# Performance work log

Measured on AMD Instinct MI355X. Metric: run time of the kernel, lower is better.

Reference implementation:

```python
import jax, jax.numpy as jnp
import numpy as np

N_NODES = 100_000
N_EDGES = 600_000
D = 128  # in_channels


def setup_inputs() -> dict:
    key = jax.random.key(0)
    k1, k2, k3, k4, k5 = jax.random.split(key, 5)
    node_embs_src = jax.random.normal(k1, (N_NODES, D), dtype=jnp.float32)
    node_embs_dst = jax.random.normal(k2, (N_NODES, D), dtype=jnp.float32)
    edge_index = jax.random.randint(k3, (2, N_EDGES), 0, N_NODES, dtype=jnp.int64)
    # MLP params: Linear(2D -> D), Linear(D -> 1); scaled like default torch init
    W1 = jax.random.normal(k4, (2 * D, D), dtype=jnp.float32) / np.sqrt(2 * D)
    b1 = jnp.zeros((D,), dtype=jnp.float32)
    W2 = jax.random.normal(k5, (D, 1), dtype=jnp.float32) / np.sqrt(D)
    b2 = jnp.zeros((1,), dtype=jnp.float32)
    return {
        "node_embs_src": node_embs_src,
        "node_embs_dst": node_embs_dst,
        "edge_index": edge_index,
        "W1": W1,
        "b1": b1,
        "W2": W2,
        "b2": b2,
    }


def reference(node_embs_src, node_embs_dst, edge_index, W1, b1, W2, b2):
    # Gather per-edge source / destination embeddings: [E, D] each
    src = node_embs_src[edge_index[0]]
    dst = node_embs_dst[edge_index[1]]
    # concat([src, dst]) @ W1 == src @ W1[:D] + dst @ W1[D:]  (avoids materializing [E, 2D])
    h = jnp.dot(src, W1[:D]) + jnp.dot(dst, W1[D:]) + b1  # [E, D]
    h = jax.nn.relu(h)
    logits = jnp.dot(h, W2) + b2  # [E, 1]
    return jax.nn.sigmoid(logits)
```

## Files before the change

kernel.cpp:

```cpp
#include <hip/hip_runtime.h>
#include <stdint.h>

typedef __attribute__((ext_vector_type(8))) short short8;
typedef __attribute__((ext_vector_type(8))) signed char schar8;
typedef __attribute__((ext_vector_type(4))) float f32x4;

__device__ __forceinline__ unsigned short f2bf(float f) {
  union { float f; uint32_t u; } v; v.f = f;
  uint32_t u = v.u;
  uint32_t r = (u + 0x7FFFu + ((u >> 16) & 1u)) >> 16;
  return (unsigned short)r;
}
__device__ __forceinline__ float bf2f(unsigned short h) {
  union { uint32_t u; float f; } v; v.u = ((uint32_t)h) << 16; return v.f;
}

#define NBM 64
__global__ __launch_bounds__(256, 3)
void node_phase_q8(const float* __restrict__ src_emb,
                   const float* __restrict__ dst_emb,
                   const float* __restrict__ W1,
                   const float* __restrict__ b1,
                   int8_t* __restrict__ Q,
                   float* __restrict__ SC,
                   int Nn, int ntiles) {
  __shared__ __align__(16) char Als[NBM * 256];
  __shared__ __align__(16) char Wlds[128 * 256];

  const int tbl = blockIdx.y;
  const float* emb = tbl ? dst_emb : src_emb;
  const float* Wt  = W1 + (size_t)tbl * 128 * 128;
  int8_t* Qt  = Q  + (size_t)tbl * Nn * 128;
  float*  SCt = SC + (size_t)tbl * Nn;

  const int tid  = threadIdx.x;
  const int lane = tid & 63;
  const int w    = tid >> 6;
  const int l15  = lane & 15;
  const int lg   = lane >> 4;

  for (int c = tid; c < 2048; c += 256) {
    const int col = c >> 4;
    const int k8  = (c & 15) * 8;
    short8 t;
#pragma unroll
    for (int j = 0; j < 8; ++j)
      t[j] = (short)f2bf(Wt[(size_t)(k8 + j) * 128 + col]);
    const int byteoff = (col * 256 + k8 * 2) ^ (((col >> 3) & 7) << 4);
    *(short8*)(Wlds + byteoff) = t;
  }

  float b1s[8];
#pragma unroll
  for (int j = 0; j < 8; ++j) b1s[j] = tbl ? 0.f : b1[l15 * 8 + j];

  const int q = tid & 15, r0 = tid >> 4;
  const int swzA = (l15 & 7) << 4;
  const int gx = gridDim.x;

  float4 p0[4], p1[4];
#pragma unroll
  for (int i = 0; i < 4; ++i) {
    const int node = blockIdx.x * NBM + i * 16 + r0;
    if (node < Nn) {
      const float* base = emb + (size_t)node * 128 + q * 8;
      p0[i] = *(const float4*)base;
      p1[i] = *(const float4*)(base + 4);
    }
  }

  for (int t = blockIdx.x; t < ntiles; t += gx) {
    const int t0 = t * NBM;

#pragma unroll
    for (int i = 0; i < 4; ++i) {
      const int row = i * 16 + r0;
      short8 hv;
      hv[0] = (short)f2bf(p0[i].x); hv[1] = (short)f2bf(p0[i].y);
      hv[2] = (short)f2bf(p0[i].z); hv[3] = (short)f2bf(p0[i].w);
      hv[4] = (short)f2bf(p1[i].x); hv[5] = (short)f2bf(p1[i].y);
      hv[6] = (short)f2bf(p1[i].z); hv[7] = (short)f2bf(p1[i].w);
      const int byteoff = row * 256 + ((q * 16) ^ ((row & 7) << 4));
      *(short8*)(Als + byteoff) = hv;
    }
    __syncthreads();

    const int tn = t + gx;
    if (tn < ntiles) {
#pragma unroll
      for (int i = 0; i < 4; ++i) {
        const int node = tn * NBM + i * 16 + r0;
        if (node < Nn) {
          const float* base = emb + (size_t)node * 128 + q * 8;
          p0[i] = *(const float4*)base;
          p1[i] = *(const float4*)(base + 4);
        }
      }
    }

    f32x4 acc[8];
#pragma unroll
    for (int cf = 0; cf < 8; ++cf) acc[cf] = (f32x4){0.f, 0.f, 0.f, 0.f};

#pragma unroll
    for (int s = 0; s < 4; ++s) {
      const int aoff = (w * 16 + l15) * 256 + ((s * 64 + lg * 16) ^ swzA);
      const short8 a = *(const short8*)(Als + aoff);
#pragma unroll
      for (int cf = 0; cf < 8; ++cf) {
        const int col = l15 * 8 + cf;
        const int boff = (col * 256 + s * 64 + lg * 16) ^ (((col >> 3) & 7) << 4);
        const short8 b = *(const short8*)(Wlds + boff);
        acc[cf] = __builtin_amdgcn_mfma_f32_16x16x32_bf16(a, b, acc[cf], 0, 0, 0);
      }
    }

#pragma unroll
    for (int reg = 0; reg < 4; ++reg) {
      float h[8];
      float am = 1e-20f;
#pragma unroll
      for (int cf = 0; cf < 8; ++cf) {
        h[cf] = acc[cf][reg] + b1s[cf];
        am = fmaxf(am, fabsf(h[cf]));
      }
      am = fmaxf(am, __shfl_xor(am, 1, 16));
      am = fmaxf(am, __shfl_xor(am, 2, 16));
      am = fmaxf(am, __shfl_xor(am, 4, 16));
      am = fmaxf(am, __shfl_xor(am, 8, 16));
      const int node = t0 + w * 16 + lg * 4 + reg;
      if (node < Nn) {
        const float rq = 127.0f / am;
        uint32_t lo = 0, hi = 0;
#pragma unroll
        for (int cf = 0; cf < 4; ++cf)
          lo |= ((uint32_t)((int)rintf(h[cf] * rq) & 255)) << (8 * cf);
#pragma unroll
        for (int cf = 4; cf < 8; ++cf)
          hi |= ((uint32_t)((int)rintf(h[cf] * rq) & 255)) << (8 * (cf - 4));
        uint2 pk; pk.x = lo; pk.y = hi;
        *(uint2*)(Qt + (size_t)node * 128 + l15 * 8) = pk;
        if (l15 == 0) SCt[node] = am * (1.0f / 127.0f);
      }
    }
    __syncthreads();
  }
}

__global__ __launch_bounds__(256, 8)
void edge_phase_q8(const int8_t* __restrict__ Qu,
                   const int8_t* __restrict__ Qv,
                   const float* __restrict__ scu,
                   const float* __restrict__ scv,
                   const int* __restrict__ eidx,
                   const float* __restrict__ W2,
                   const float* __restrict__ b2,
                   float* __restrict__ out,
                   int E) {
  const int tid = threadIdx.x;
  const int l15 = tid & 15;
  const int sg  = tid >> 4;

  float w2s[8];
#pragma unroll
  for (int j = 0; j < 8; ++j) w2s[j] = W2[l15 * 8 + j];
  const float b2s = b2[0];
  const int stride = gridDim.x * 16;

#pragma unroll 2
  for (int e = blockIdx.x * 16 + sg; e < E; e += stride) {
    const int s = eidx[e];
    const int d = eidx[E + e];
    const schar8 qu = *(const schar8*)(Qu + (size_t)s * 128 + l15 * 8);
    const schar8 qv = *(const schar8*)(Qv + (size_t)d * 128 + l15 * 8);
    const float su = scu[s];
    const float sv = scv[d];
    float acc = 0.f;
#pragma unroll
    for (int j = 0; j < 8; ++j) {
      float g = (float)(int)qu[j] * su + (float)(int)qv[j] * sv;
      g = g > 0.f ? g : 0.f;
      acc = fmaf(g, w2s[j], acc);
    }
    acc += __shfl_xor(acc, 1, 16);
    acc += __shfl_xor(acc, 2, 16);
    acc += __shfl_xor(acc, 4, 16);
    acc += __shfl_xor(acc, 8, 16);
    if (l15 == 0) out[e] = 1.f / (1.f + __expf(-(acc + b2s)));
  }
}

#define BM 64
__global__ __launch_bounds__(256, 4)
void edge_decoder_fused(const float* __restrict__ src_emb,
                        const float* __restrict__ dst_emb,
                        const int* __restrict__ eidx,
                        const float* __restrict__ W1,
                        const float* __restrict__ b1,
                        const float* __restrict__ W2,
                        const float* __restrict__ b2,
                        float* __restrict__ out,
                        int E, int ntiles) {
  __shared__ __align__(16) char Als[BM * 512];
  __shared__ float rowpart[4][BM];

  const int tid  = threadIdx.x;
  const int lane = tid & 63;
  const int w    = tid >> 6;
  const int l15  = lane & 15;
  const int lk8  = (lane >> 4) * 8;

  short8 bfrag[8][2];
#pragma unroll
  for (int s = 0; s < 8; ++s) {
#pragma unroll
    for (int nf = 0; nf < 2; ++nf) {
      const int col = w * 32 + nf * 16 + l15;
      short8 t;
#pragma unroll
      for (int j = 0; j < 8; ++j) {
        const int k = s * 32 + lk8 + j;
        t[j] = (short)f2bf(W1[k * 128 + col]);
      }
      bfrag[s][nf] = t;
    }
  }
  float b1v[2], w2v[2];
#pragma unroll
  for (int nf = 0; nf < 2; ++nf) {
    const int col = w * 32 + nf * 16 + l15;
    b1v[nf] = b1[col];
    w2v[nf] = W2[col];
  }
  const float b2s = b2[0];

  const int q  = tid & 31;
  const int r0 = tid >> 5;
  const int qq = q & 15;
  const bool is_src = (q < 16);
  const int swz = (l15 & 7) << 4;

  for (int t = blockIdx.x; t < ntiles; t += gridDim.x) {
    const int t0 = t * BM;
#pragma unroll
    for (int i = 0; i < 8; ++i) {
      const int row = i * 8 + r0;
      const int e = t0 + row;
      if (e < E) {
        const int node = is_src ? eidx[e] : eidx[E + e];
        const float* base = (is_src ? src_emb : dst_emb) + (size_t)node * 128 + qq * 8;
        const float4 f0 = *(const float4*)base;
        const float4 f1 = *(const float4*)(base + 4);
        short8 hv;
        hv[0] = (short)f2bf(f0.x); hv[1] = (short)f2bf(f0.y);
        hv[2] = (short)f2bf(f0.z); hv[3] = (short)f2bf(f0.w);
        hv[4] = (short)f2bf(f1.x); hv[5] = (short)f2bf(f1.y);
        hv[6] = (short)f2bf(f1.z); hv[7] = (short)f2bf(f1.w);
        const int byteoff = row * 512 + ((q * 16) ^ ((row & 7) << 4));
        *(short8*)(Als + byteoff) = hv;
      }
    }
    __syncthreads();

    for (int m = 0; m < 4; ++m) {
      f32x4 acc0 = {0.f, 0.f, 0.f, 0.f};
      f32x4 acc1 = {0.f, 0.f, 0.f, 0.f};
      const int rowb = (m * 16 + l15) * 512;
      const int kb0  = lk8 * 2;
#pragma unroll
      for (int s = 0; s < 8; ++s) {
        const int off = rowb + ((s * 64 + kb0) ^ swz);
        const short8 a = *(const short8*)(Als + off);
        acc0 = __builtin_amdgcn_mfma_f32_16x16x32_bf16(a, bfrag[s][0], acc0, 0, 0, 0);
        acc1 = __builtin_amdgcn_mfma_f32_16x16x32_bf16(a, bfrag[s][1], acc1, 0, 0, 0);
      }
      float pr[4];
#pragma unroll
      for (int reg = 0; reg < 4; ++reg) {
        float h0 = acc0[reg] + b1v[0]; h0 = h0 > 0.f ? h0 : 0.f;
        float h1 = acc1[reg] + b1v[1]; h1 = h1 > 0.f ? h1 : 0.f;
        pr[reg] = h0 * w2v[0] + h1 * w2v[1];
      }
#pragma unroll
      for (int off = 1; off < 16; off <<= 1) {
#pragma unroll
        for (int reg = 0; reg < 4; ++reg)
          pr[reg] += __shfl_xor(pr[reg], off, 64);
      }
      if (l15 == 0) {
        const int rbase = m * 16 + (lane >> 4) * 4;
#pragma unroll
        for (int reg = 0; reg < 4; ++reg)
          rowpart[w][rbase + reg] = pr[reg];
      }
    }
    __syncthreads();

    if (tid < BM) {
      const int e = t0 + tid;
      if (e < E) {
        const float sum = rowpart[0][tid] + rowpart[1][tid] +
                          rowpart[2][tid] + rowpart[3][tid] + b2s;
        out[e] = 1.f / (1.f + __expf(-sum));
      }
    }
    __syncthreads();
  }
}

extern "C" void kernel_launch(void* const* d_in, const int* in_sizes, int n_in,
                              void* d_out, int out_size, void* d_ws, size_t ws_size,
                              hipStream_t stream) {
  const float* src = (const float*)d_in[0];
  const float* dst = (const float*)d_in[1];
  const int*   eix = (const int*)d_in[2];
  const float* W1  = (const float*)d_in[3];
  const float* b1  = (const float*)d_in[4];
  const float* W2  = (const float*)d_in[5];
  const float* b2  = (const float*)d_in[6];
  float* out = (float*)d_out;

  const int E  = in_sizes[2] / 2;
  const int Nn = in_sizes[0] / 128;
  const size_t q_bytes  = (size_t)2 * Nn * 128;
  const size_t sc_bytes = (size_t)2 * Nn * sizeof(float);

  if (ws_size >= q_bytes + sc_bytes) {
    int8_t* Q  = (int8_t*)d_ws;
    float*  SC = (float*)((char*)d_ws + q_bytes);
    const int ntiles_n = (Nn + NBM - 1) / NBM;
    const int gx = ntiles_n < 384 ? ntiles_n : 384;
    node_phase_q8<<<dim3(gx, 2), 256, 0, stream>>>(src, dst, W1, b1, Q, SC, Nn, ntiles_n);
    const int nchunks = (E + 15) / 16;
    const int nblk = nchunks < 2048 ? nchunks : 2048;
    edge_phase_q8<<<nblk, 256, 0, stream>>>(Q, Q + (size_t)Nn * 128, SC, SC + Nn,
                                            eix, W2, b2, out, E);
  } else {
    const int ntiles = (E + BM - 1) / BM;
    const int grid = ntiles < 2048 ? ntiles : 2048;
    edge_decoder_fused<<<grid, 256, 0, stream>>>(src, dst, eix, W1, b1, W2, b2,
                                                 out, E, ntiles);
  }
}
```

Before: 75.62 us.

## Hold W1 fragments in registers, transpose MFMA roles, move bias to edge phase

The node-phase GEMM now keeps the bf16 W1 operand in per-wave registers (afrag) instead of LDS, swapping MFMA A/B roles so each lane owns one node row and writes contiguous 32-byte quantized chunks. Per-row absmax now needs only two cross-lane shuffles, and the LDS weight tile is gone, removing its per-iteration reads. The b1 bias moves out of the quantized node activations into the edge phase as an extra FMA. In exchange register pressure rises sharply (128 VGPRs of weights), so occupancy is lowered to 2 and the grid to 256 blocks per table. Quantization error shifts because the quantized values no longer include the bias.

```diff
diff --git a/kernel.cpp b/kernel.cpp
--- a/kernel.cpp
+++ b/kernel.cpp
@@ -16,16 +16,14 @@
 }
 
 #define NBM 64
-__global__ __launch_bounds__(256, 3)
+__global__ __launch_bounds__(256, 2)
 void node_phase_q8(const float* __restrict__ src_emb,
                    const float* __restrict__ dst_emb,
                    const float* __restrict__ W1,
-                   const float* __restrict__ b1,
                    int8_t* __restrict__ Q,
                    float* __restrict__ SC,
                    int Nn, int ntiles) {
   __shared__ __align__(16) char Als[NBM * 256];
-  __shared__ __align__(16) char Wlds[128 * 256];
 
   const int tbl = blockIdx.y;
   const float* emb = tbl ? dst_emb : src_emb;
@@ -39,23 +37,23 @@
   const int l15  = lane & 15;
   const int lg   = lane >> 4;
 
-  for (int c = tid; c < 2048; c += 256) {
-    const int col = c >> 4;
-    const int k8  = (c & 15) * 8;
-    short8 t;
-#pragma unroll
-    for (int j = 0; j < 8; ++j)
-      t[j] = (short)f2bf(Wt[(size_t)(k8 + j) * 128 + col]);
-    const int byteoff = (col * 256 + k8 * 2) ^ (((col >> 3) & 7) << 4);
-    *(short8*)(Wlds + byteoff) = t;
-  }
-
-  float b1s[8];
-#pragma unroll
-  for (int j = 0; j < 8; ++j) b1s[j] = tbl ? 0.f : b1[l15 * 8 + j];
+  const int pbase = (l15 >> 2) * 32 + (l15 & 3);
+  short8 afrag[8][4];
+#pragma unroll
+  for (int m = 0; m < 8; ++m) {
+#pragma unroll
+    for (int s = 0; s < 4; ++s) {
+      short8 t;
+#pragma unroll
+      for (int j = 0; j < 8; ++j) {
+        const int k = s * 32 + lg * 8 + j;
+        t[j] = (short)f2bf(Wt[(size_t)k * 128 + pbase + m * 4]);
+      }
+      afrag[m][s] = t;
+    }
+  }
 
   const int q = tid & 15, r0 = tid >> 4;
-  const int swzA = (l15 & 7) << 4;
   const int gx = gridDim.x;
 
   float4 p0[4], p1[4];
@@ -100,48 +98,46 @@
 
     f32x4 acc[8];
 #pragma unroll
-    for (int cf = 0; cf < 8; ++cf) acc[cf] = (f32x4){0.f, 0.f, 0.f, 0.f};
-
+    for (int m = 0; m < 8; ++m) acc[m] = (f32x4){0.f, 0.f, 0.f, 0.f};
+
+    const int brow = w * 16 + l15;
+    const int bswz = (l15 & 7) << 4;
 #pragma unroll
     for (int s = 0; s < 4; ++s) {
-      const int aoff = (w * 16 + l15) * 256 + ((s * 64 + lg * 16) ^ swzA);
-      const short8 a = *(const short8*)(Als + aoff);
-#pragma unroll
-      for (int cf = 0; cf < 8; ++cf) {
-        const int col = l15 * 8 + cf;
-        const int boff = (col * 256 + s * 64 + lg * 16) ^ (((col >> 3) & 7) << 4);
-        const short8 b = *(const short8*)(Wlds + boff);
-        acc[cf] = __builtin_amdgcn_mfma_f32_16x16x32_bf16(a, b, acc[cf], 0, 0, 0);
-      }
-    }
-
-#pragma unroll
-    for (int reg = 0; reg < 4; ++reg) {
-      float h[8];
-      float am = 1e-20f;
-#pragma unroll
-      for (int cf = 0; cf < 8; ++cf) {
-        h[cf] = acc[cf][reg] + b1s[cf];
-        am = fmaxf(am, fabsf(h[cf]));
-      }
-      am = fmaxf(am, __shfl_xor(am, 1, 16));
-      am = fmaxf(am, __shfl_xor(am, 2, 16));
-      am = fmaxf(am, __shfl_xor(am, 4, 16));
-      am = fmaxf(am, __shfl_xor(am, 8, 16));
-      const int node = t0 + w * 16 + lg * 4 + reg;
-      if (node < Nn) {
-        const float rq = 127.0f / am;
-        uint32_t lo = 0, hi = 0;
-#pragma unroll
-        for (int cf = 0; cf < 4; ++cf)
-          lo |= ((uint32_t)((int)rintf(h[cf] * rq) & 255)) << (8 * cf);
-#pragma unroll
-        for (int cf = 4; cf < 8; ++cf)
-          hi |= ((uint32_t)((int)rintf(h[cf] * rq) & 255)) << (8 * (cf - 4));
-        uint2 pk; pk.x = lo; pk.y = hi;
-        *(uint2*)(Qt + (size_t)node * 128 + l15 * 8) = pk;
-        if (l15 == 0) SCt[node] = am * (1.0f / 127.0f);
-      }
+      const int boff = brow * 256 + ((s * 64 + lg * 16) ^ bswz);
+      const short8 b = *(const short8*)(Als + boff);
+#pragma unroll
+      for (int m = 0; m < 8; ++m)
+        acc[m] = __builtin_amdgcn_mfma_f32_16x16x32_bf16(afrag[m][s], b, acc[m], 0, 0, 0);
+    }
+
+    float am = 1e-20f;
+#pragma unroll
+    for (int m = 0; m < 8; ++m)
+#pragma unroll
+      for (int reg = 0; reg < 4; ++reg)
+        am = fmaxf(am, fabsf(acc[m][reg]));
+    am = fmaxf(am, __shfl_xor(am, 16));
+    am = fmaxf(am, __shfl_xor(am, 32));
+
+    const int node = t0 + w * 16 + l15;
+    if (node < Nn) {
+      const float rq = 127.0f / am;
+      uint32_t d[8];
+#pragma unroll
+      for (int m = 0; m < 8; ++m) {
+        uint32_t pk = 0;
+#pragma unroll
+        for (int reg = 0; reg < 4; ++reg)
+          pk |= ((uint32_t)((int)rintf(acc[m][reg] * rq) & 255)) << (8 * reg);
+        d[m] = pk;
+      }
+      uint4 lo; lo.x = d[0]; lo.y = d[1]; lo.z = d[2]; lo.w = d[3];
+      uint4 hi; hi.x = d[4]; hi.y = d[5]; hi.z = d[6]; hi.w = d[7];
+      int8_t* dst = Qt + (size_t)node * 128 + lg * 32;
+      *(uint4*)dst        = lo;
+      *(uint4*)(dst + 16) = hi;
+      if (lg == 0) SCt[node] = am * (1.0f / 127.0f);
     }
     __syncthreads();
   }
@@ -153,6 +149,7 @@
                    const float* __restrict__ scu,
                    const float* __restrict__ scv,
                    const int* __restrict__ eidx,
+                   const float* __restrict__ b1,
                    const float* __restrict__ W2,
                    const float* __restrict__ b2,
                    float* __restrict__ out,
@@ -161,9 +158,12 @@
   const int l15 = tid & 15;
   const int sg  = tid >> 4;
 
-  float w2s[8];
-#pragma unroll
-  for (int j = 0; j < 8; ++j) w2s[j] = W2[l15 * 8 + j];
+  float w2s[8], b1s[8];
+#pragma unroll
+  for (int j = 0; j < 8; ++j) {
+    w2s[j] = W2[l15 * 8 + j];
+    b1s[j] = b1[l15 * 8 + j];
+  }
   const float b2s = b2[0];
   const int stride = gridDim.x * 16;
 
@@ -178,7 +178,8 @@
     float acc = 0.f;
 #pragma unroll
     for (int j = 0; j < 8; ++j) {
-      float g = (float)(int)qu[j] * su + (float)(int)qv[j] * sv;
+      float g = fmaf((float)(int)qu[j], su,
+                fmaf((float)(int)qv[j], sv, b1s[j]));
       g = g > 0.f ? g : 0.f;
       acc = fmaf(g, w2s[j], acc);
     }
@@ -329,12 +330,12 @@
     int8_t* Q  = (int8_t*)d_ws;
     float*  SC = (float*)((char*)d_ws + q_bytes);
     const int ntiles_n = (Nn + NBM - 1) / NBM;
-    const int gx = ntiles_n < 384 ? ntiles_n : 384;
-    node_phase_q8<<<dim3(gx, 2), 256, 0, stream>>>(src, dst, W1, b1, Q, SC, Nn, ntiles_n);
+    const int gx = ntiles_n < 256 ? ntiles_n : 256;
+    node_phase_q8<<<dim3(gx, 2), 256, 0, stream>>>(src, dst, W1, Q, SC, Nn, ntiles_n);
     const int nchunks = (E + 15) / 16;
     const int nblk = nchunks < 2048 ? nchunks : 2048;
     edge_phase_q8<<<nblk, 256, 0, stream>>>(Q, Q + (size_t)Nn * 128, SC, SC + Nn,
-                                            eix, W2, b2, out, E);
+                                            eix, b1, W2, b2, out, E);
   } else {
     const int ntiles = (E + BM - 1) / BM;
     const int grid = ntiles < 2048 ? ntiles : 2048;
```

Measured after the change: 98.86 us. 1.31x slower.
